# Kernel tuning notes

Hardware: AMD Instinct MI355X
Metric: run time of the kernel (lower is better)

The kernel has to match this reference:

```python
import jax, jax.numpy as jnp
import numpy as np

N, E, FEAT, DIM, B = 200000, 1600000, 128, 64, 256


def setup_inputs() -> dict:
    key = jax.random.key(0)
    ks = jax.random.split(key, 16)
    s = 0.05
    x = jax.random.normal(ks[0], (N, FEAT), jnp.float32)
    edge_index = jax.random.randint(ks[1], (2, E), 0, N)
    batch = jnp.sort(jax.random.randint(ks[2], (N,), 0, B))
    return {
        'x': x,
        'edge_index': edge_index,
        'batch': batch,
        'lin0_w': jax.random.normal(ks[3], (FEAT, DIM), jnp.float32) * s,
        'lin0_b': jax.random.normal(ks[4], (DIM,), jnp.float32) * s,
        'conv_w': jax.random.normal(ks[5], (DIM, DIM), jnp.float32) * s,
        'conv_b': jax.random.normal(ks[6], (DIM,), jnp.float32) * s,
        'gru_w_ih': jax.random.normal(ks[7], (3 * DIM, DIM), jnp.float32) * s,
        'gru_w_hh': jax.random.normal(ks[8], (3 * DIM, DIM), jnp.float32) * s,
        'gru_b_ih': jax.random.normal(ks[9], (3 * DIM,), jnp.float32) * s,
        'gru_b_hh': jax.random.normal(ks[10], (3 * DIM,), jnp.float32) * s,
        'lstm_w_ih': jax.random.normal(ks[11], (4 * DIM, 2 * DIM), jnp.float32) * s,
        'lstm_w_hh': jax.random.normal(ks[12], (4 * DIM, DIM), jnp.float32) * s,
        'lstm_b_ih': jax.random.normal(ks[13], (4 * DIM,), jnp.float32) * s,
        'lstm_b_hh': jax.random.normal(ks[14], (4 * DIM,), jnp.float32) * s,
    }


def reference(x, edge_index, batch, lin0_w, lin0_b, conv_w, conv_b,
              gru_w_ih, gru_w_hh, gru_b_ih, gru_b_hh,
              lstm_w_ih, lstm_w_hh, lstm_b_ih, lstm_b_hh):
    n = x.shape[0]
    d = lin0_w.shape[1]
    # --- GCN normalization with self-loops (PyG gcn_norm, symmetric) ---
    loops = jnp.arange(n)
    row = jnp.concatenate([edge_index[0], loops])  # source nodes
    col = jnp.concatenate([edge_index[1], loops])  # target nodes
    deg = jax.ops.segment_sum(jnp.ones(row.shape, jnp.float32), col, num_segments=N)
    dinv = jnp.where(deg > 0, jax.lax.rsqrt(deg), 0.0)
    norm = dinv[row] * dinv[col]  # [E+N]

    out = jax.nn.relu(x @ lin0_w + lin0_b)  # [N, D]
    h = out  # GRU hidden (layer dim squeezed)
    feat = out
    for _ in range(3):
        # GCNConv: aggregate normalized neighbor messages
        hw = out @ conv_w                                   # [N, D]
        m = jax.ops.segment_sum(norm[:, None] * hw[row], col, num_segments=N) + conv_b
        m = jax.nn.relu(m)
        # torch.nn.GRU cell (gate order: reset, update, new)
        gi = m @ gru_w_ih.T + gru_b_ih
        gh = h @ gru_w_hh.T + gru_b_hh
        ir, iz, in_ = jnp.split(gi, 3, axis=-1)
        hr, hz, hn = jnp.split(gh, 3, axis=-1)
        r = jax.nn.sigmoid(ir + hr)
        z = jax.nn.sigmoid(iz + hz)
        ncand = jnp.tanh(in_ + r * hn)
        h = (1.0 - z) * ncand + z * h
        out = h
        feat = out

    # --- Set2Set pooling, processing_steps=3 (LSTM: 2D -> D) ---
    q_star = jnp.zeros((B, 2 * d), x.dtype)
    hl = jnp.zeros((B, d), x.dtype)
    cl = jnp.zeros((B, d), x.dtype)
    for _ in range(3):
        gates = q_star @ lstm_w_ih.T + lstm_b_ih + hl @ lstm_w_hh.T + lstm_b_hh
        i_, f_, g_, o_ = jnp.split(gates, 4, axis=-1)  # torch order i,f,g,o
        cl = jax.nn.sigmoid(f_) * cl + jax.nn.sigmoid(i_) * jnp.tanh(g_)
        hl = jax.nn.sigmoid(o_) * jnp.tanh(cl)
        q = hl                                             # [B, D]
        e = jnp.sum(out * q[batch], axis=-1)               # [N]
        emax = jax.ops.segment_max(e, batch, num_segments=B)
        a = jnp.exp(e - jax.lax.stop_gradient(emax)[batch])
        denom = jax.ops.segment_sum(a, batch, num_segments=B)
        a = a / denom[batch]                               # scatter-softmax
        r_read = jax.ops.segment_sum(a[:, None] * out, batch, num_segments=B)
        q_star = jnp.concatenate([q, r_read], axis=-1)     # [B, 2D]
    return (q_star, feat)
```

## Files before the change

### kernel.cpp

```cpp
#include <hip/hip_runtime.h>
#include <math.h>

#define FEATD 128
#define DIM 64
#define NB 256
#define SCB 256
#define KB 16
#define RNG 128
#define NBUCKMAX 2048
#define CH1 8192

typedef short bf16x8 __attribute__((ext_vector_type(8)));
typedef float f32x4 __attribute__((ext_vector_type(4)));

__device__ __forceinline__ float frcp_(float x){ return __builtin_amdgcn_rcpf(x); }
__device__ __forceinline__ float sigmoidf_(float x){ return frcp_(1.f+__expf(-x)); }
__device__ __forceinline__ float tanhf_(float x){ float e=__expf(2.f*x); return 1.f-2.f*frcp_(e+1.f); }

__device__ __forceinline__ unsigned short f2bf(float f){
  unsigned u = __float_as_uint(f);
  unsigned r = (u + 0x7FFFu + ((u>>16)&1u)) >> 16;
  return (unsigned short)r;
}
__device__ __forceinline__ float bf2f(unsigned short s){
  return __uint_as_float(((unsigned)s)<<16);
}

__device__ __forceinline__ int lower_bound_i(const int* __restrict__ a, int n, int key){
  int lo=0, hi=n;
  while(lo<hi){ int mid=(lo+hi)>>1; if(a[mid]<key) lo=mid+1; else hi=mid; }
  return lo;
}

__global__ void k_count(const int* __restrict__ col, int* __restrict__ deg, int E){
  int i=blockIdx.x*blockDim.x+threadIdx.x;
  if(i<E) atomicAdd(&deg[col[i]],1);
}

__global__ __launch_bounds__(256) void k_scan_part(const int* __restrict__ deg, int* __restrict__ part,
                                                   float* __restrict__ dinv, int n){
  __shared__ int s[256];
  int b=blockIdx.x;
  int chunk=(n+SCB-1)/SCB;
  int lo=b*chunk, hi=min(lo+chunk,n);
  int acc=0;
  for(int i=lo+threadIdx.x;i<hi;i+=256){
    int d=deg[i];
    acc+=d;
    dinv[i]=rsqrtf((float)(d+1));
  }
  s[threadIdx.x]=acc; __syncthreads();
  for(int off=128;off;off>>=1){
    if(threadIdx.x<off) s[threadIdx.x]+=s[threadIdx.x+off];
    __syncthreads();
  }
  if(threadIdx.x==0) part[b]=s[0];
}

__global__ __launch_bounds__(256) void k_scan_mid(int* __restrict__ part){
  __shared__ int s[256];
  int t=threadIdx.x;
  s[t]=part[t]; __syncthreads();
  for(int off=1;off<256;off<<=1){
    int v=(t>=off)? s[t-off]:0;
    __syncthreads();
    s[t]+=v;
    __syncthreads();
  }
  part[t]=(t>0)? s[t-1]:0;
}

__global__ __launch_bounds__(256) void k_scan_out(const int* __restrict__ deg, const int* __restrict__ part,
                                                  int* __restrict__ rp, int* __restrict__ gcur, int n){
  __shared__ int s[256];
  int b=blockIdx.x, t=threadIdx.x;
  int chunk=(n+SCB-1)/SCB;
  int lo=b*chunk, hi=min(lo+chunk,n);
  int tchunk=(chunk+255)/256;
  int tlo=lo+t*tchunk, thi=min(tlo+tchunk,hi);
  int acc=0;
  for(int i=tlo;i<thi;i++) acc+=deg[i];
  s[t]=acc; __syncthreads();
  for(int off=1;off<256;off<<=1){
    int v=(t>=off)? s[t-off]:0;
    __syncthreads();
    s[t]+=v;
    __syncthreads();
  }
  int pre=part[b]+((t>0)? s[t-1]:0);
  for(int i=tlo;i<thi;i++){
    rp[i]=pre;
    if((i&(RNG-1))==0) gcur[(i>>7)*32]=pre;
    pre+=deg[i];
  }
  if(b==SCB-1 && t==0) rp[n]=part[b]+s[255];
}

__global__ __launch_bounds__(256) void k_binscat(const int* __restrict__ row, const int* __restrict__ col,
                       int* __restrict__ gcur, unsigned* __restrict__ tmp, int E, int nbuck){
  __shared__ int lcnt[NBUCKMAX];
  __shared__ int lcur[NBUCKMAX];
  int t=threadIdx.x;
  for(int i=t;i<nbuck;i+=256) lcnt[i]=0;
  __syncthreads();
  int lo=blockIdx.x*CH1, hi=min(lo+CH1,E);
  for(int i=lo+t;i<hi;i+=256) atomicAdd(&lcnt[col[i]>>7],1);
  __syncthreads();
  for(int i=t;i<nbuck;i+=256){
    int cnt=lcnt[i];
    lcur[i]=(cnt>0)? atomicAdd(&gcur[i*32],cnt):0;
  }
  __syncthreads();
  for(int i=lo+t;i<hi;i+=256){
    int c=col[i], r=row[i];
    int pos=atomicAdd(&lcur[c>>7],1);
    tmp[pos]=((unsigned)r<<7)|(unsigned)(c&127);
  }
}

__global__ __launch_bounds__(256) void k_place(const unsigned* __restrict__ tmp, const int* __restrict__ rp,
                      const float* __restrict__ dinv, int2* __restrict__ epack, int n, int nbuck){
  __shared__ int lfill[RNG];
  __shared__ int lrp[RNG];
  __shared__ float ldv[RNG];
  int b=blockIdx.x, t=threadIdx.x;
  int nbase=b*RNG;
  int nn=min(RNG,n-nbase);
  if(t<nn){ lfill[t]=0; lrp[t]=rp[nbase+t]; ldv[t]=dinv[nbase+t]; }
  __syncthreads();
  int lo=rp[nbase], hi=rp[min(nbase+RNG,n)];
  for(int j=lo+t;j<hi;j+=256){
    unsigned v=tmp[j];
    int cl=v&127;
    int r=(int)(v>>7);
    int pos=atomicAdd(&lfill[cl],1);
    epack[lrp[cl]+pos]=make_int2(r,__float_as_int(dinv[r]*ldv[cl]));
  }
}

__global__ void k_prep_plain(const float* __restrict__ W, unsigned short* __restrict__ Bf, int K, int C){
  int i=blockIdx.x*blockDim.x+threadIdx.x;
  if(i>=K*C) return;
  int k=i/C, c=i%C;
  int t=c>>4, s=k>>5, lane=(c&15)|(((k>>3)&3)<<4), r=k&7;
  int S=K>>5;
  Bf[(((t*S)+s)*64+lane)*8+r]=f2bf(W[(size_t)k*C+c]);
}

__global__ void k_prep_gru(const float* __restrict__ wih, const float* __restrict__ whh,
                           unsigned short* __restrict__ Bf){
  int i=blockIdx.x*blockDim.x+threadIdx.x;
  if(i>=128*256) return;
  int k=i>>8, c=i&255;
  float v;
  if(c<128){
    v = (k<64) ? wih[c*64+k] : whh[c*64+(k-64)];
  } else if(c<192){
    v = (k<64) ? wih[c*64+k] : 0.f;
  } else {
    v = (k<64) ? 0.f : whh[(c-64)*64+(k-64)];
  }
  int t=c>>4, s=k>>5, lane=(c&15)|(((k>>3)&3)<<4), r=k&7;
  Bf[(((s*16)+t)*64+lane)*8+r]=f2bf(v);
}

__global__ __launch_bounds__(256) void k_lin0(const float* __restrict__ x, const unsigned short* __restrict__ Bf,
                      const float* __restrict__ bias,
                      unsigned short* __restrict__ hb, int ngrp){
  __shared__ __align__(16) unsigned short lt[4][16][72];
  int l=threadIdx.x&63, w=threadIdx.x>>6;
  int g=blockIdx.x*4+w;
  if(g>=ngrp) return;
  int row16=l&15, koff=(l>>4)*8, l16=l&15;
  f32x4 acc[4]={};
  const float* xr = x + (size_t)(g*16+row16)*128 + koff;
  #pragma unroll
  for(int s=0;s<4;s++){
    f32x4 a0=*(const f32x4*)(xr+s*32);
    f32x4 a1=*(const f32x4*)(xr+s*32+4);
    bf16x8 af;
    #pragma unroll
    for(int r=0;r<4;r++){ af[r]=(short)f2bf(a0[r]); af[4+r]=(short)f2bf(a1[r]); }
    #pragma unroll
    for(int t=0;t<4;t++){
      bf16x8 bf=*(const bf16x8*)(Bf+(((t*4)+s)*64+l)*8);
      acc[t]=__builtin_amdgcn_mfma_f32_16x16x32_bf16(af,bf,acc[t],0,0,0);
    }
  }
  #pragma unroll
  for(int t=0;t<4;t++){
    int c=t*16+l16;
    float b=bias[c];
    #pragma unroll
    for(int j=0;j<4;j++)
      lt[w][(l>>4)*4+j][c]=f2bf(fmaxf(acc[t][j]+b,0.f));
  }
  #pragma unroll
  for(int i=0;i<4;i++){
    int rl=i*4+(l>>4);
    uint2 v=*(const uint2*)&lt[w][rl][l16*4];
    ((uint2*)hb)[(((unsigned)(g*16+rl))<<4)+l16]=v;
  }
}

__global__ __launch_bounds__(256,4) void k_gruagg(
                     const unsigned short* __restrict__ hin, unsigned short* __restrict__ hout,
                     const int* __restrict__ rp, const int2* __restrict__ epack,
                     const float* __restrict__ dinv,
                     const unsigned short* __restrict__ Bcnv, const float* __restrict__ cb,
                     const unsigned short* __restrict__ Bgru,
                     const float* __restrict__ bih, const float* __restrict__ bhh,
                     float* __restrict__ h, int last, int ngrp, int n){
  __shared__ __align__(16) unsigned short Bs[8192];
  __shared__ __align__(16) unsigned short tAH[4][2][16][72];
  int tid=threadIdx.x;
  int l=tid&63, w=tid>>6;
  int g=blockIdx.x*4+w;
  bool act = g<ngrp;
  int gc = act? g : (ngrp-1);
  int q=l>>4, l16=l&15;
  int row16=l&15, koff=(l>>4)*8;

  unsigned short (*tA)[72] = tAH[w][0];
  unsigned short (*tH)[72] = tAH[w][1];

  bf16x8 bc[8];
  #pragma unroll
  for(int f=0;f<8;f++) bc[f]=*(const bf16x8*)(Bcnv+((size_t)f*64+l)*8);

  {
    const f32x4* gh=(const f32x4*)Bgru; f32x4* lh=(f32x4*)Bs;
    #pragma unroll
    for(int i=0;i<4;i++) lh[i*256+tid]=gh[i*256+tid];
  }

  const uint2* h64=(const uint2*)hin;
  #pragma unroll
  for(int rr=0;rr<4;rr++){
    int node=min(gc*16+rr*4+q, n-1);
    float a0=0.f,a1=0.f,a2=0.f,a3=0.f, b0=0.f,b1=0.f,b2=0.f,b3=0.f;
    int s=rp[node], e=rp[node+1];
    uint2 selfp=h64[((unsigned)node<<4)+l16];
    int j=s;
    for(; j+7<e; j+=8){
      int2 e0=epack[j],   e1=epack[j+1], e2=epack[j+2], e3=epack[j+3];
      int2 e4=epack[j+4], e5=epack[j+5], e6=epack[j+6], e7=epack[j+7];
      uint2 p0=h64[((unsigned)e0.x<<4)+l16];
      uint2 p1=h64[((unsigned)e1.x<<4)+l16];
      uint2 p2=h64[((unsigned)e2.x<<4)+l16];
      uint2 p3=h64[((unsigned)e3.x<<4)+l16];
      uint2 p4=h64[((unsigned)e4.x<<4)+l16];
      uint2 p5=h64[((unsigned)e5.x<<4)+l16];
      uint2 p6=h64[((unsigned)e6.x<<4)+l16];
      uint2 p7=h64[((unsigned)e7.x<<4)+l16];
      float n0=__int_as_float(e0.y), n1=__int_as_float(e1.y);
      float n2=__int_as_float(e2.y), n3=__int_as_float(e3.y);
      float n4=__int_as_float(e4.y), n5=__int_as_float(e5.y);
      float n6=__int_as_float(e6.y), n7=__int_as_float(e7.y);
      a0+=n0*bf2f((unsigned short)p0.x); a1+=n0*bf2f((unsigned short)(p0.x>>16));
      a2+=n0*bf2f((unsigned short)p0.y); a3+=n0*bf2f((unsigned short)(p0.y>>16));
      b0+=n1*bf2f((unsigned short)p1.x); b1+=n1*bf2f((unsigned short)(p1.x>>16));
      b2+=n1*bf2f((unsigned short)p1.y); b3+=n1*bf2f((unsigned short)(p1.y>>16));
      a0+=n2*bf2f((unsigned short)p2.x); a1+=n2*bf2f((unsigned short)(p2.x>>16));
      a2+=n2*bf2f((unsigned short)p2.y); a3+=n2*bf2f((unsigned short)(p2.y>>16));
      b0+=n3*bf2f((unsigned short)p3.x); b1+=n3*bf2f((unsigned short)(p3.x>>16));
      b2+=n3*bf2f((unsigned short)p3.y); b3+=n3*bf2f((unsigned short)(p3.y>>16));
      a0+=n4*bf2f((unsigned short)p4.x); a1+=n4*bf2f((unsigned short)(p4.x>>16));
      a2+=n4*bf2f((unsigned short)p4.y); a3+=n4*bf2f((unsigned short)(p4.y>>16));
      b0+=n5*bf2f((unsigned short)p5.x); b1+=n5*bf2f((unsigned short)(p5.x>>16));
      b2+=n5*bf2f((unsigned short)p5.y); b3+=n5*bf2f((unsigned short)(p5.y>>16));
      a0+=n6*bf2f((unsigned short)p6.x); a1+=n6*bf2f((unsigned short)(p6.x>>16));
      a2+=n6*bf2f((unsigned short)p6.y); a3+=n6*bf2f((unsigned short)(p6.y>>16));
      b0+=n7*bf2f((unsigned short)p7.x); b1+=n7*bf2f((unsigned short)(p7.x>>16));
      b2+=n7*bf2f((unsigned short)p7.y); b3+=n7*bf2f((unsigned short)(p7.y>>16));
    }
    for(; j+3<e; j+=4){
      int2 e0=epack[j];
      int2 e1=epack[j+1];
      int2 e2=epack[j+2];
      int2 e3=epack[j+3];
      uint2 p0=h64[((unsigned)e0.x<<4)+l16];
      uint2 p1=h64[((unsigned)e1.x<<4)+l16];
      uint2 p2=h64[((unsigned)e2.x<<4)+l16];
      uint2 p3=h64[((unsigned)e3.x<<4)+l16];
      float n0=__int_as_float(e0.y), n1=__int_as_float(e1.y);
      float n2=__int_as_float(e2.y), n3=__int_as_float(e3.y);
      a0+=n0*bf2f((unsigned short)p0.x); a1+=n0*bf2f((unsigned short)(p0.x>>16));
      a2+=n0*bf2f((unsigned short)p0.y); a3+=n0*bf2f((unsigned short)(p0.y>>16));
      b0+=n1*bf2f((unsigned short)p1.x); b1+=n1*bf2f((unsigned short)(p1.x>>16));
      b2+=n1*bf2f((unsigned short)p1.y); b3+=n1*bf2f((unsigned short)(p1.y>>16));
      a0+=n2*bf2f((unsigned short)p2.x); a1+=n2*bf2f((unsigned short)(p2.x>>16));
      a2+=n2*bf2f((unsigned short)p2.y); a3+=n2*bf2f((unsigned short)(p2.y>>16));
      b0+=n3*bf2f((unsigned short)p3.x); b1+=n3*bf2f((unsigned short)(p3.x>>16));
      b2+=n3*bf2f((unsigned short)p3.y); b3+=n3*bf2f((unsigned short)(p3.y>>16));
    }
    for(; j+1<e; j+=2){
      int2 e0=epack[j];
      int2 e1=epack[j+1];
      uint2 p0=h64[((unsigned)e0.x<<4)+l16];
      uint2 p1=h64[((unsigned)e1.x<<4)+l16];
      float n0=__int_as_float(e0.y), n1=__int_as_float(e1.y);
      a0+=n0*bf2f((unsigned short)p0.x); a1+=n0*bf2f((unsigned short)(p0.x>>16));
      a2+=n0*bf2f((unsigned short)p0.y); a3+=n0*bf2f((unsigned short)(p0.y>>16));
      b0+=n1*bf2f((unsigned short)p1.x); b1+=n1*bf2f((unsigned short)(p1.x>>16));
      b2+=n1*bf2f((unsigned short)p1.y); b3+=n1*bf2f((unsigned short)(p1.y>>16));
    }
    if(j<e){
      int2 e0=epack[j];
      uint2 p0=h64[((unsigned)e0.x<<4)+l16];
      float n0=__int_as_float(e0.y);
      a0+=n0*bf2f((unsigned short)p0.x); a1+=n0*bf2f((unsigned short)(p0.x>>16));
      a2+=n0*bf2f((unsigned short)p0.y); a3+=n0*bf2f((unsigned short)(p0.y>>16));
    }
    float dv=dinv[node]; dv*=dv;
    a0+=b0+dv*bf2f((unsigned short)selfp.x);
    a1+=b1+dv*bf2f((unsigned short)(selfp.x>>16));
    a2+=b2+dv*bf2f((unsigned short)selfp.y);
    a3+=b3+dv*bf2f((unsigned short)(selfp.y>>16));
    int ri=rr*4+q;
    unsigned* tAp=(unsigned*)&tA[ri][l16*4];
    tAp[0]=(unsigned)f2bf(a0)|(((unsigned)f2bf(a1))<<16);
    tAp[1]=(unsigned)f2bf(a2)|(((unsigned)f2bf(a3))<<16);
    unsigned* tHp=(unsigned*)&tH[ri][l16*4];
    tHp[0]=selfp.x; tHp[1]=selfp.y;
  }

  f32x4 accm[4]={};
  #pragma unroll
  for(int s=0;s<2;s++){
    bf16x8 af=*(const bf16x8*)&tA[row16][s*32+koff];
    #pragma unroll
    for(int t=0;t<4;t++)
      accm[t]=__builtin_amdgcn_mfma_f32_16x16x32_bf16(af,bc[t*2+s],accm[t],0,0,0);
  }
  #pragma unroll
  for(int t=0;t<4;t++){
    int c=t*16+l16;
    float b=cb[c];
    #pragma unroll
    for(int j=0;j<4;j++)
      tA[(l>>4)*4+j][c]=f2bf(fmaxf(accm[t][j]+b,0.f));
  }

  f32x4 acc[16]={};
  __syncthreads();
  #pragma unroll
  for(int s=0;s<4;s++){
    if(s>0){
      __syncthreads();
      const f32x4* gh=(const f32x4*)(Bgru+(size_t)s*8192); f32x4* lh=(f32x4*)Bs;
      #pragma unroll
      for(int i=0;i<4;i++) lh[i*256+tid]=gh[i*256+tid];
      __syncthreads();
    }
    bf16x8 af;
    if(s<2) af=*(const bf16x8*)&tA[row16][s*32+koff];
    else    af=*(const bf16x8*)&tH[row16][(s-2)*32+koff];
    #pragma unroll
    for(int t=0;t<16;t++){
      bf16x8 bf=*(const bf16x8*)(Bs+((size_t)t*64+l)*8);
      acc[t]=__builtin_amdgcn_mfma_f32_16x16x32_bf16(af,bf,acc[t],0,0,0);
    }
  }

  if(!act) return;
  float hn[16];
  #pragma unroll
  for(int t=0;t<4;t++){
    int d=t*16+l16;
    float br =bih[d]    +bhh[d];
    float bz =bih[64+d] +bhh[64+d];
    float bni=bih[128+d];
    float bnh=bhh[128+d];
    #pragma unroll
    for(int j=0;j<4;j++){
      float r  = sigmoidf_(acc[t][j]   + br);
      float z  = sigmoidf_(acc[4+t][j] + bz);
      float nc = tanhf_(acc[8+t][j] + bni + r*(acc[12+t][j] + bnh));
      float hold=bf2f(tH[(l>>4)*4+j][d]);
      hn[t*4+j]=(1.f-z)*nc + z*hold;
    }
  }
  #pragma unroll
  for(int t=0;t<4;t++){
    int d=t*16+l16;
    #pragma unroll
    for(int j=0;j<4;j++)
      tH[(l>>4)*4+j][d]=f2bf(hn[t*4+j]);
  }
  #pragma unroll
  for(int i=0;i<4;i++){
    int rl=i*4+(l>>4);
    uint2 v=*(const uint2*)&tH[rl][l16*4];
    ((uint2*)hout)[(((unsigned)(gc*16+rl))<<4)+l16]=v;
  }
  if(last){
    float* ft=(float*)&tAH[w][0][0][0];
    #pragma unroll
    for(int t=0;t<4;t++){
      int d=t*16+l16;
      #pragma unroll
      for(int j=0;j<4;j++)
        ft[((l>>4)*4+j)*68+d]=hn[t*4+j];
    }
    #pragma unroll
    for(int i=0;i<4;i++){
      int rl=i*4+(l>>4);
      f32x4 v=*(const f32x4*)&ft[rl*68+l16*4];
      *(f32x4*)&h[(size_t)(gc*16+rl)*64+l16*4]=v;
    }
  }
}

__global__ __launch_bounds__(256) void k_attn_part(const unsigned short* __restrict__ hb, const int* __restrict__ batch,
                        const float* __restrict__ hl, float* __restrict__ apart, int n){
  int b=blockIdx.x/KB, kb=blockIdx.x%KB;
  int tid=threadIdx.x, lane=tid&63, w=tid>>6;
  __shared__ float qs[64];
  __shared__ float wm[4], wsm[4];
  __shared__ float wacc[4][64];
  if(tid<64) qs[tid]=hl[b*64+tid];
  int lo=lower_bound_i(batch,n,b), hi=lower_bound_i(batch,n,b+1);
  int cnt=hi-lo;
  int chunk=(cnt+KB-1)/KB;
  int slo=lo+kb*chunk, shi=min(slo+chunk,hi);
  __syncthreads();
  float q=qs[lane];
  float mw=-3.0e38f, sw=0.f, aw=0.f;
  for(int i=slo+w;i<shi;i+=4){
    float f=bf2f(hb[(size_t)i*64+lane]);
    float v=f*q;
    #pragma unroll
    for(int off=32;off;off>>=1) v+=__shfl_xor(v,off);
    if(v>mw){
      float sc=__expf(mw-v);
      sw=sw*sc+1.f;
      aw=aw*sc+f;
      mw=v;
    } else {
      float p=__expf(v-mw);
      sw+=p;
      aw+=p*f;
    }
  }
  if(lane==0){ wm[w]=mw; wsm[w]=sw; }
  wacc[w][lane]=aw;
  __syncthreads();
  if(w==0){
    float M=fmaxf(fmaxf(wm[0],wm[1]),fmaxf(wm[2],wm[3]));
    float S=0.f, A=0.f;
    #pragma unroll
    for(int k=0;k<4;k++){
      float sc=__expf(wm[k]-M);
      S+=wsm[k]*sc;
      A+=wacc[k][lane]*sc;
    }
    float* p=apart+(size_t)blockIdx.x*68;
    p[lane]=A;
    if(lane==0){ p[64]=M; p[65]=S; }
  }
}

__global__ __launch_bounds__(256) void k_merge_lstm(const float* __restrict__ apart,
                   float* __restrict__ qstar, float* __restrict__ hl, float* __restrict__ cl,
                   const float* __restrict__ wih, const float* __restrict__ whh,
                   const float* __restrict__ bih, const float* __restrict__ bhh,
                   int do_merge, int do_lstm){
  int b=blockIdx.x, tid=threadIdx.x;
  __shared__ float qs[128];
  __shared__ float gates[256];
  if(do_merge){
    if(tid<64){
      const float* p0=apart+(size_t)b*KB*68;
      float M=-3.0e38f;
      #pragma unroll
      for(int k=0;k<KB;k++) M=fmaxf(M,p0[k*68+64]);
      float S=0.f, A=0.f;
      #pragma unroll
      for(int k=0;k<KB;k++){
        float sc=__expf(p0[k*68+64]-M);
        S+=p0[k*68+65]*sc;
        A+=p0[k*68+tid]*sc;
      }
      float inv=(S>0.f)? 1.f/S:0.f;
      float r=A*inv;
      qs[64+tid]=r;
      qstar[b*128+64+tid]=r;
    }
  } else {
    if(tid<64) qs[64+tid]=qstar[b*128+64+tid];
  }
  if(tid<64) qs[tid]=hl[b*64+tid];
  __syncthreads();
  if(!do_lstm) return;
  float acc=bih[tid]+bhh[tid];
  const float* wi=wih+(size_t)tid*128;
  #pragma unroll 8
  for(int k=0;k<128;k++) acc+=qs[k]*wi[k];
  const float* w2=whh+(size_t)tid*64;
  #pragma unroll 8
  for(int k=0;k<64;k++) acc+=qs[k]*w2[k];
  gates[tid]=acc;
  __syncthreads();
  if(tid<64){
    float i_=gates[tid], f_=gates[64+tid], g_=gates[128+tid], o_=gates[192+tid];
    float c=sigmoidf_(f_)*cl[b*64+tid]+sigmoidf_(i_)*tanhf(g_);
    float hn=sigmoidf_(o_)*tanhf(c);
    cl[b*64+tid]=c; hl[b*64+tid]=hn;
    qstar[b*128+tid]=hn;
  }
}

extern "C" void kernel_launch(void* const* d_in, const int* in_sizes, int n_in,
                              void* d_out, int out_size, void* d_ws, size_t ws_size,
                              hipStream_t stream){
  const float* x      =(const float*)d_in[0];
  const int*   ei     =(const int*)d_in[1];
  const int*   batch  =(const int*)d_in[2];
  const float* lin0_w =(const float*)d_in[3];
  const float* lin0_b =(const float*)d_in[4];
  const float* conv_w =(const float*)d_in[5];
  const float* conv_b =(const float*)d_in[6];
  const float* gwih   =(const float*)d_in[7];
  const float* gwhh   =(const float*)d_in[8];
  const float* gbih   =(const float*)d_in[9];
  const float* gbhh   =(const float*)d_in[10];
  const float* lwih   =(const float*)d_in[11];
  const float* lwhh   =(const float*)d_in[12];
  const float* lbih   =(const float*)d_in[13];
  const float* lbhh   =(const float*)d_in[14];

  int N = in_sizes[0]/FEATD;
  int E = in_sizes[1]/2;
  const int* row = ei;
  const int* col = ei + E;

  float* qstar = (float*)d_out;
  float* h     = (float*)d_out + NB*2*DIM;

  char* ws=(char*)d_ws;
  size_t off=0;
  auto alloc=[&](size_t bytes)->void*{ void* p=ws+off; off=(off+bytes+255)&~(size_t)255; return p; };
  int*   deg  =(int*)  alloc((size_t)N*4);
  float* dinv =(float*)alloc((size_t)N*4);
  int*   rp   =(int*)  alloc((size_t)(N+1)*4);
  int*   part =(int*)  alloc((size_t)SCB*4);
  int*   gcur =(int*)  alloc((size_t)NBUCKMAX*32*4);
  unsigned* tmp=(unsigned*)alloc((size_t)E*4);
  int2*  epack=(int2*) alloc((size_t)E*8);
  unsigned short* hb0  =(unsigned short*)alloc((size_t)N*64*2);
  unsigned short* hb1  =(unsigned short*)alloc((size_t)N*64*2);
  float* hl   =(float*)alloc((size_t)NB*DIM*4);
  float* cl   =(float*)alloc((size_t)NB*DIM*4);
  float* apart=(float*)alloc((size_t)NB*KB*68*4);
  unsigned short* Bgru =(unsigned short*)alloc(128*256*2);
  unsigned short* Blin =(unsigned short*)alloc(128*64*2);
  unsigned short* Bcnv =(unsigned short*)alloc(64*64*2);

  hipMemsetAsync(deg ,0,(size_t)N*4,stream);
  hipMemsetAsync(hl  ,0,(size_t)NB*DIM*4,stream);
  hipMemsetAsync(cl  ,0,(size_t)NB*DIM*4,stream);
  hipMemsetAsync(qstar,0,(size_t)NB*2*DIM*4,stream);

  int nbuck=(N+RNG-1)/RNG;

  k_count<<<(E+255)/256,256,0,stream>>>(col,deg,E);
  k_scan_part<<<SCB,256,0,stream>>>(deg,part,dinv,N);
  k_scan_mid <<<1,256,0,stream>>>(part);
  k_scan_out <<<SCB,256,0,stream>>>(deg,part,rp,gcur,N);
  k_binscat<<<(E+CH1-1)/CH1,256,0,stream>>>(row,col,gcur,tmp,E,nbuck);
  k_place<<<nbuck,256,0,stream>>>(tmp,rp,dinv,epack,N,nbuck);

  k_prep_plain<<<(128*64+255)/256,256,0,stream>>>(lin0_w,Blin,128,64);
  k_prep_plain<<<(64*64+255)/256,256,0,stream>>>(conv_w,Bcnv,64,64);
  k_prep_gru  <<<(128*256+255)/256,256,0,stream>>>(gwih,gwhh,Bgru);

  int ngrp=(N+15)/16;
  int gb=(ngrp+3)/4;

  k_lin0<<<gb,256,0,stream>>>(x,Blin,lin0_b,hb0,ngrp);

  k_gruagg<<<gb,256,0,stream>>>(hb0,hb1,rp,epack,dinv,Bcnv,conv_b,Bgru,gbih,gbhh,h,0,ngrp,N);
  k_gruagg<<<gb,256,0,stream>>>(hb1,hb0,rp,epack,dinv,Bcnv,conv_b,Bgru,gbih,gbhh,h,0,ngrp,N);
  k_gruagg<<<gb,256,0,stream>>>(hb0,hb1,rp,epack,dinv,Bcnv,conv_b,Bgru,gbih,gbhh,h,1,ngrp,N);

  k_merge_lstm<<<NB,256,0,stream>>>(apart,qstar,hl,cl,lwih,lwhh,lbih,lbhh,0,1);
  for(int st=0;st<3;st++){
    k_attn_part<<<NB*KB,256,0,stream>>>(hb1,batch,hl,apart,N);
    int do_lstm = (st<2)? 1:0;
    k_merge_lstm<<<NB,256,0,stream>>>(apart,qstar,hl,cl,lwih,lwhh,lbih,lbhh,1,do_lstm);
  }
}
```

Before: 538.8 us.

## Sort nodes by in-degree to balance per-lane neighbor loops in GRU aggregation

Builds a degree histogram during the scan pass and turns it into prefix offsets. A new kernel then places node ids into a permutation grouped by in-degree. The fused GCN+GRU kernel processes nodes in that order, so lanes sharing a wavefront walk neighbor lists of similar length, which cuts divergence and tail imbalance. In exchange it adds an extra launch with heavily contended global atomics on a few bins, an indirection load per node, and scattered (non-contiguous) row writes of the hidden state and the final output.

```diff
diff --git a/kernel.cpp b/kernel.cpp
--- a/kernel.cpp
+++ b/kernel.cpp
@@ -9,6 +9,7 @@
 #define RNG 128
 #define NBUCKMAX 2048
 #define CH1 8192
+#define DB 64
 
 typedef short bf16x8 __attribute__((ext_vector_type(8)));
 typedef float f32x4 __attribute__((ext_vector_type(4)));
@@ -38,9 +39,12 @@
 }
 
 __global__ __launch_bounds__(256) void k_scan_part(const int* __restrict__ deg, int* __restrict__ part,
-                                                   float* __restrict__ dinv, int n){
+                                                   float* __restrict__ dinv, int* __restrict__ dhist, int n){
   __shared__ int s[256];
+  __shared__ int lh[DB];
   int b=blockIdx.x;
+  if(threadIdx.x<DB) lh[threadIdx.x]=0;
+  __syncthreads();
   int chunk=(n+SCB-1)/SCB;
   int lo=b*chunk, hi=min(lo+chunk,n);
   int acc=0;
@@ -48,6 +52,7 @@
     int d=deg[i];
     acc+=d;
     dinv[i]=rsqrtf((float)(d+1));
+    atomicAdd(&lh[min(d,DB-1)],1);
   }
   s[threadIdx.x]=acc; __syncthreads();
   for(int off=128;off;off>>=1){
@@ -55,9 +60,10 @@
     __syncthreads();
   }
   if(threadIdx.x==0) part[b]=s[0];
-}
-
-__global__ __launch_bounds__(256) void k_scan_mid(int* __restrict__ part){
+  if(threadIdx.x<DB && lh[threadIdx.x]>0) atomicAdd(&dhist[threadIdx.x],lh[threadIdx.x]);
+}
+
+__global__ __launch_bounds__(256) void k_scan_mid(int* __restrict__ part, int* __restrict__ dhist){
   __shared__ int s[256];
   int t=threadIdx.x;
   s[t]=part[t]; __syncthreads();
@@ -68,6 +74,18 @@
     __syncthreads();
   }
   part[t]=(t>0)? s[t-1]:0;
+  if(t==0){
+    int run=0;
+    for(int i=0;i<DB;i++){ int v=dhist[i]; dhist[i]=run; run+=v; }
+  }
+}
+
+__global__ void k_dplace(const int* __restrict__ deg, int* __restrict__ dhist, int* __restrict__ perm, int n){
+  int i=blockIdx.x*blockDim.x+threadIdx.x;
+  if(i>=n) return;
+  int b=min(deg[i],DB-1);
+  int pos=atomicAdd(&dhist[b],1);
+  perm[pos]=i;
 }
 
 __global__ __launch_bounds__(256) void k_scan_out(const int* __restrict__ deg, const int* __restrict__ part,
@@ -206,7 +224,7 @@
 __global__ __launch_bounds__(256,4) void k_gruagg(
                      const unsigned short* __restrict__ hin, unsigned short* __restrict__ hout,
                      const int* __restrict__ rp, const int2* __restrict__ epack,
-                     const float* __restrict__ dinv,
+                     const float* __restrict__ dinv, const int* __restrict__ perm,
                      const unsigned short* __restrict__ Bcnv, const float* __restrict__ cb,
                      const unsigned short* __restrict__ Bgru,
                      const float* __restrict__ bih, const float* __restrict__ bhh,
@@ -237,7 +255,7 @@
   const uint2* h64=(const uint2*)hin;
   #pragma unroll
   for(int rr=0;rr<4;rr++){
-    int node=min(gc*16+rr*4+q, n-1);
+    int node=perm[min(gc*16+rr*4+q, n-1)];
     float a0=0.f,a1=0.f,a2=0.f,a3=0.f, b0=0.f,b1=0.f,b2=0.f,b3=0.f;
     int s=rp[node], e=rp[node+1];
     uint2 selfp=h64[((unsigned)node<<4)+l16];
@@ -391,8 +409,9 @@
   #pragma unroll
   for(int i=0;i<4;i++){
     int rl=i*4+(l>>4);
+    int node=perm[gc*16+rl];
     uint2 v=*(const uint2*)&tH[rl][l16*4];
-    ((uint2*)hout)[(((unsigned)(gc*16+rl))<<4)+l16]=v;
+    ((uint2*)hout)[(((unsigned)node<<4))+l16]=v;
   }
   if(last){
     float* ft=(float*)&tAH[w][0][0][0];
@@ -406,8 +425,9 @@
     #pragma unroll
     for(int i=0;i<4;i++){
       int rl=i*4+(l>>4);
+      int node=perm[gc*16+rl];
       f32x4 v=*(const f32x4*)&ft[rl*68+l16*4];
-      *(f32x4*)&h[(size_t)(gc*16+rl)*64+l16*4]=v;
+      *(f32x4*)&h[(size_t)node*64+l16*4]=v;
     }
   }
 }
@@ -546,6 +566,8 @@
   int*   rp   =(int*)  alloc((size_t)(N+1)*4);
   int*   part =(int*)  alloc((size_t)SCB*4);
   int*   gcur =(int*)  alloc((size_t)NBUCKMAX*32*4);
+  int*   dhist=(int*)  alloc((size_t)DB*4);
+  int*   perm =(int*)  alloc((size_t)N*4);
   unsigned* tmp=(unsigned*)alloc((size_t)E*4);
   int2*  epack=(int2*) alloc((size_t)E*8);
   unsigned short* hb0  =(unsigned short*)alloc((size_t)N*64*2);
@@ -558,6 +580,7 @@
   unsigned short* Bcnv =(unsigned short*)alloc(64*64*2);
 
   hipMemsetAsync(deg ,0,(size_t)N*4,stream);
+  hipMemsetAsync(dhist,0,(size_t)DB*4,stream);
   hipMemsetAsync(hl  ,0,(size_t)NB*DIM*4,stream);
   hipMemsetAsync(cl  ,0,(size_t)NB*DIM*4,stream);
   hipMemsetAsync(qstar,0,(size_t)NB*2*DIM*4,stream);
@@ -565,8 +588,9 @@
   int nbuck=(N+RNG-1)/RNG;
 
   k_count<<<(E+255)/256,256,0,stream>>>(col,deg,E);
-  k_scan_part<<<SCB,256,0,stream>>>(deg,part,dinv,N);
-  k_scan_mid <<<1,256,0,stream>>>(part);
+  k_scan_part<<<SCB,256,0,stream>>>(deg,part,dinv,dhist,N);
+  k_scan_mid <<<1,256,0,stream>>>(part,dhist);
+  k_dplace<<<(N+255)/256,256,0,stream>>>(deg,dhist,perm,N);
   k_scan_out <<<SCB,256,0,stream>>>(deg,part,rp,gcur,N);
   k_binscat<<<(E+CH1-1)/CH1,256,0,stream>>>(row,col,gcur,tmp,E,nbuck);
   k_place<<<nbuck,256,0,stream>>>(tmp,rp,dinv,epack,N,nbuck);
@@ -580,9 +604,9 @@
 
   k_lin0<<<gb,256,0,stream>>>(x,Blin,lin0_b,hb0,ngrp);
 
-  k_gruagg<<<gb,256,0,stream>>>(hb0,hb1,rp,epack,dinv,Bcnv,conv_b,Bgru,gbih,gbhh,h,0,ngrp,N);
-  k_gruagg<<<gb,256,0,stream>>>(hb1,hb0,rp,epack,dinv,Bcnv,conv_b,Bgru,gbih,gbhh,h,0,ngrp,N);
-  k_gruagg<<<gb,256,0,stream>>>(hb0,hb1,rp,epack,dinv,Bcnv,conv_b,Bgru,gbih,gbhh,h,1,ngrp,N);
+  k_gruagg<<<gb,256,0,stream>>>(hb0,hb1,rp,epack,dinv,perm,Bcnv,conv_b,Bgru,gbih,gbhh,h,0,ngrp,N);
+  k_gruagg<<<gb,256,0,stream>>>(hb1,hb0,rp,epack,dinv,perm,Bcnv,conv_b,Bgru,gbih,gbhh,h,0,ngrp,N);
+  k_gruagg<<<gb,256,0,stream>>>(hb0,hb1,rp,epack,dinv,perm,Bcnv,conv_b,Bgru,gbih,gbhh,h,1,ngrp,N);
 
   k_merge_lstm<<<NB,256,0,stream>>>(apart,qstar,hl,cl,lwih,lwhh,lbih,lbhh,0,1);
   for(int st=0;st<3;st++){
```

After: 1.212 ms. +124.9%, slower.
